# Kernel tuning notes

Hardware: AMD Instinct MI355X
Metric: run time of the kernel (lower is better)

The kernel has to match this reference:

```python
import jax, jax.numpy as jnp
import numpy as np

DIM = 1024
HEADS = 16
DIM_HEAD = 64
B = 16
N = 512
INNER = HEADS * DIM_HEAD            # 1024
CPB_DIM = DIM // 2                  # 512
INNER_FF = int(DIM * 4 * 2 / 3)     # 2730
EPS = 1e-5


def setup_inputs() -> dict:
    key = jax.random.key(0)
    ks = jax.random.split(key, 10)
    s = lambda i, shape, scale: jax.random.normal(ks[i], shape, jnp.float32) * scale
    return dict(
        x=s(0, (B, N, DIM), 1.0),
        g_ln=jnp.ones((DIM,), jnp.float32),
        Wq=s(1, (DIM, INNER), 0.02),
        Wkv=s(2, (DIM, 2 * INNER), 0.02),
        Wo=s(3, (INNER, DIM), 0.02),
        cpb_w1=s(4, (1, CPB_DIM), 0.5),
        cpb_b1=jnp.zeros((CPB_DIM,), jnp.float32),
        cpb_w2=s(5, (CPB_DIM, CPB_DIM), 0.05),
        cpb_b2=jnp.zeros((CPB_DIM,), jnp.float32),
        cpb_w3=s(6, (CPB_DIM, HEADS), 0.05),
        cpb_b3=jnp.zeros((HEADS,), jnp.float32),
        ff_w_in=s(7, (2 * INNER_FF, DIM), 0.02),
        ff_g=jnp.ones((INNER_FF,), jnp.float32),
        ff_w_out=s(8, (DIM, INNER_FF), 0.02),
    )


def _seq_ln(x, g):
    # Faithful to repo's LayerNorm: mean/var over dim=1 (sequence axis of [b,n,d])
    mean = jnp.mean(x, axis=1, keepdims=True)
    var = jnp.var(x, axis=1, keepdims=True)  # unbiased=False
    return (x - mean) * jax.lax.rsqrt(jnp.maximum(var, EPS)) * g


def reference(x, g_ln, Wq, Wkv, Wo, cpb_w1, cpb_b1, cpb_w2, cpb_b2, cpb_w3, cpb_b3,
              ff_w_in, ff_g, ff_w_out):
    b, n, d = x.shape
    # ContinuousPositionBias (1D, 2 layers)
    pos = jnp.arange(n, dtype=jnp.float32)
    rel = (pos[:, None] - pos[None, :])[..., None]           # [n,n,1]
    rel = jnp.sign(rel) * jnp.log(jnp.abs(rel) + 1.0)        # log-distance
    h = jax.nn.silu(rel @ cpb_w1 + cpb_b1)
    h = jax.nn.silu(h @ cpb_w2 + cpb_b2)
    bias = (h @ cpb_w3 + cpb_b3).transpose(2, 0, 1)          # [h,n,n]

    # Attention (framerate=None -> no pos_embeds; context = x)
    xn = _seq_ln(x, g_ln)
    q = xn @ Wq
    k, v = jnp.split(xn @ Wkv, 2, axis=-1)
    to_heads = lambda t: t.reshape(b, n, HEADS, DIM_HEAD).transpose(0, 2, 1, 3)
    q, k, v = to_heads(q), to_heads(k), to_heads(v)
    q = q * (DIM_HEAD ** -0.5)
    sim = jnp.einsum('bhid,bhjd->bhij', q, k) + bias[None]
    attn = jax.nn.softmax(sim, axis=-1)
    o = jnp.einsum('bhij,bhjd->bhid', attn, v)
    o = o.transpose(0, 2, 1, 3).reshape(b, n, INNER)
    x = jnp.nan_to_num(o @ Wo) + x

    # FeedForward: Conv1d(k=1) -> GEGLU -> ChanLayerNorm -> Conv1d(k=1), residual
    xt = x.transpose(0, 2, 1)                                # [b,d,n]
    hff = jnp.einsum('oc,bcn->bon', ff_w_in, xt)             # [b,2*inner_ff,n]
    x1, gate = jnp.split(hff, 2, axis=1)
    hff = x1 * jax.nn.gelu(gate, approximate=False)
    mean = jnp.mean(hff, axis=1, keepdims=True)
    var = jnp.var(hff, axis=1, keepdims=True)
    hff = (hff - mean) * jax.lax.rsqrt(jnp.maximum(var, EPS)) * ff_g[None, :, None]
    out = jnp.einsum('oc,bcn->bon', ff_w_out, hff).transpose(0, 2, 1) + x
    return out
```

## Files before the change

### kernel.cpp

```cpp
#include <hip/hip_runtime.h>

#define DEV __device__ __forceinline__

typedef __attribute__((ext_vector_type(8))) short bf16x8;
typedef __attribute__((ext_vector_type(4))) float f32x4;
typedef __attribute__((ext_vector_type(16))) float f32x16;

DEV float b2f(unsigned short u) { union { unsigned int i; float f; } v; v.i = ((unsigned)u) << 16; return v.f; }
DEV unsigned short f2b(float f) {
    union { float f; unsigned int i; } v; v.f = f;
    unsigned r = v.i + 0x7FFFu + ((v.i >> 16) & 1u);
    return (unsigned short)(r >> 16);
}

DEV void llds16(const unsigned short* g, unsigned short* l) {
    __builtin_amdgcn_global_load_lds((const __attribute__((address_space(1))) void*)g,
                                     (__attribute__((address_space(3))) void*)l, 16, 0, 0);
}

DEV float gelu_f(float x) {
    float y = 0.7978845608f * (x + 0.044715f * x * x * x);
    float th = 1.f - 2.f / (__expf(2.f * y) + 1.f);
    return 0.5f * x * (1.f + th);
}

__global__ __launch_bounds__(256) void transpose_cast_k(const float* __restrict__ src,
        unsigned short* __restrict__ dst, int Nc, int K, float scale)
{
    __shared__ float tile[32][33];
    int tx = threadIdx.x, ty = threadIdx.y;
    int c0 = blockIdx.x * 32;
    int r0 = blockIdx.y * 32;
#pragma unroll
    for (int r = 0; r < 4; r++)
        tile[ty + r * 8][tx] = src[(size_t)(r0 + ty + r * 8) * Nc + c0 + tx];
    __syncthreads();
#pragma unroll
    for (int r = 0; r < 4; r++)
        dst[(size_t)(c0 + ty + r * 8) * K + r0 + tx] = f2b(tile[tx][ty + r * 8] * scale);
}

__global__ __launch_bounds__(256) void cast_wfin_k(const float* __restrict__ src,
        unsigned short* __restrict__ dst)
{
    int idx = blockIdx.x * 256 + threadIdx.x;
    int nr = idx >> 8;
    int c4 = (idx & 255) * 4;
    int chunk = nr >> 6, which = (nr >> 5) & 1, pos = nr & 31;
    int c = chunk * 32 + pos;
    unsigned short o0 = 0, o1 = 0, o2 = 0, o3 = 0;
    if (c < 2730) {
        const float* s = src + (size_t)(which * 2730 + c) * 1024 + c4;
        o0 = f2b(s[0]); o1 = f2b(s[1]); o2 = f2b(s[2]); o3 = f2b(s[3]);
    }
    unsigned short* d = dst + (size_t)nr * 1024 + c4;
    d[0] = o0; d[1] = o1; d[2] = o2; d[3] = o3;
}

__global__ __launch_bounds__(256) void cast_wfoutg_k(const float* __restrict__ src,
        const float* __restrict__ g, unsigned short* __restrict__ dst)
{
    int idx = blockIdx.x * 256 + threadIdx.x;
    int r = idx / 2752, c = idx % 2752;
    float v = (c < 2730) ? src[(size_t)r * 2730 + c] * g[c] : 0.f;
    dst[idx] = f2b(v);
}

__global__ __launch_bounds__(64) void wgsum_k(const float* __restrict__ w,
        const float* __restrict__ g, float* __restrict__ wgs)
{
    int o = blockIdx.x, t = threadIdx.x;
    float s = 0.f;
    for (int c = t; c < 2730; c += 64) s += w[(size_t)o * 2730 + c] * g[c];
#pragma unroll
    for (int off = 32; off > 0; off >>= 1) s += __shfl_xor(s, off);
    if (t == 0) wgs[o] = s;
}

__global__ __launch_bounds__(512) void cpb_k(const float* __restrict__ w1, const float* __restrict__ b1,
        const float* __restrict__ w2, const float* __restrict__ b2,
        const float* __restrict__ w3, const float* __restrict__ b3,
        float* __restrict__ btbl)
{
    __shared__ float sH[512];
    __shared__ float sH2[512];
    int t = threadIdx.x, row = blockIdx.x;
    int dd = row - 511;
    float ad = fabsf((float)dd);
    float sgn = (dd > 0) ? 1.f : ((dd < 0) ? -1.f : 0.f);
    float rel = sgn * logf(ad + 1.f);
    float h1 = rel * w1[t] + b1[t];
    h1 = h1 / (1.f + __expf(-h1));
    sH[t] = h1;
    __syncthreads();
    float a = b2[t];
    for (int k = 0; k < 512; k++) a += sH[k] * w2[(size_t)k * 512 + t];
    a = a / (1.f + __expf(-a));
    sH2[t] = a;
    __syncthreads();
    if (t < 16) {
        float s = b3[t];
        for (int k = 0; k < 512; k++) s += sH2[k] * w3[k * 16 + t];
        btbl[t * 1023 + row] = s;
    }
}

__global__ __launch_bounds__(256) void ln_stat_k(const float* __restrict__ x,
        float* __restrict__ part_s, float* __restrict__ part_q)
{
    int b = blockIdx.x >> 4, nc = blockIdx.x & 15, t = threadIdx.x;
    const float* xp = x + ((size_t)b * 512 + nc * 32) * 1024;
#pragma unroll
    for (int dc = 0; dc < 4; dc++) {
        int d = dc * 256 + t;
        float s = 0.f, q = 0.f;
#pragma unroll 8
        for (int n = 0; n < 32; n++) { float v = xp[(size_t)n * 1024 + d]; s += v; q += v * v; }
        part_s[((size_t)b * 16 + nc) * 1024 + d] = s;
        part_q[((size_t)b * 16 + nc) * 1024 + d] = q;
    }
}

__global__ __launch_bounds__(256) void ln_reduce_k(const float* __restrict__ part_s,
        const float* __restrict__ part_q, const float* __restrict__ gln,
        float* __restrict__ mean, float* __restrict__ inv)
{
    int b = blockIdx.x >> 2, d = (blockIdx.x & 3) * 256 + threadIdx.x;
    float s = 0.f, q = 0.f;
#pragma unroll
    for (int c = 0; c < 16; c++) {
        s += part_s[((size_t)b * 16 + c) * 1024 + d];
        q += part_q[((size_t)b * 16 + c) * 1024 + d];
    }
    float m = s * (1.f / 512.f);
    float var = q * (1.f / 512.f) - m * m;
    mean[b * 1024 + d] = m;
    inv[b * 1024 + d] = rsqrtf(fmaxf(var, 1e-5f)) * gln[d];
}

__global__ __launch_bounds__(256) void ln_apply_k(const float* __restrict__ x,
        const float* __restrict__ mean, const float* __restrict__ inv,
        unsigned short* __restrict__ xn)
{
    int b = blockIdx.x >> 4, nc = blockIdx.x & 15, t = threadIdx.x;
    const float* xp = x + ((size_t)b * 512 + nc * 32) * 1024;
    unsigned short* op = xn + ((size_t)b * 512 + nc * 32) * 1024;
#pragma unroll
    for (int dc = 0; dc < 4; dc++) {
        int d = dc * 256 + t;
        float m = mean[b * 1024 + d], iv = inv[b * 1024 + d];
#pragma unroll 8
        for (int n = 0; n < 32; n++)
            op[(size_t)n * 1024 + d] = f2b((xp[(size_t)n * 1024 + d] - m) * iv);
    }
}

__global__ __launch_bounds__(256) void gemm_bt128_k(const unsigned short* __restrict__ A,
        const unsigned short* __restrict__ BT, unsigned short* __restrict__ C,
        float* __restrict__ OUTF, const float* __restrict__ RESF,
        const unsigned short* __restrict__ RESB,
        const float* __restrict__ MU, const float* __restrict__ INVV,
        const float* __restrict__ WGS, int K, int ldc, int mode)
{
    __shared__ __align__(16) unsigned short lds[16384];
    int t = threadIdx.x, lane = t & 63, w = t >> 6;
    int m0 = blockIdx.x * 128, n0 = blockIdx.y * 128;
    int wm = (w >> 1) * 64, wn = (w & 1) * 64;
    int lm = lane & 15, lq = lane >> 4;
    int srow = t >> 2, scol = (t & 3) * 8;
    const unsigned short* gA0 = A + (size_t)(m0 + srow) * K + scol;
    const unsigned short* gB0 = BT + (size_t)(n0 + srow) * K + scol;
    const size_t rstep = (size_t)64 * K;
    int wb = w * 512;

    f32x4 acc[4][4];
#pragma unroll
    for (int i = 0; i < 4; i++)
#pragma unroll
        for (int j = 0; j < 4; j++) acc[i][j] = (f32x4){0.f, 0.f, 0.f, 0.f};

    for (int kk = 0; kk < K; kk += 64) {
        __syncthreads();
        llds16(gA0 + kk,              &lds[wb]);
        llds16(gA0 + rstep + kk,      &lds[2048 + wb]);
        llds16(gB0 + kk,              &lds[4096 + wb]);
        llds16(gB0 + rstep + kk,      &lds[6144 + wb]);
        llds16(gA0 + kk + 32,         &lds[8192 + wb]);
        llds16(gA0 + rstep + kk + 32, &lds[10240 + wb]);
        llds16(gB0 + kk + 32,         &lds[12288 + wb]);
        llds16(gB0 + rstep + kk + 32, &lds[14336 + wb]);
        __syncthreads();
#pragma unroll
        for (int p = 0; p < 2; p++) {
            int pa = p * 8192, pb = p * 8192 + 4096;
            bf16x8 af[4], bfr[4];
#pragma unroll
            for (int i = 0; i < 4; i++) af[i] = *(const bf16x8*)&lds[pa + (wm + i * 16 + lm) * 32 + lq * 8];
#pragma unroll
            for (int j = 0; j < 4; j++) bfr[j] = *(const bf16x8*)&lds[pb + (wn + j * 16 + lm) * 32 + lq * 8];
#pragma unroll
            for (int i = 0; i < 4; i++)
#pragma unroll
                for (int j = 0; j < 4; j++)
                    acc[i][j] = __builtin_amdgcn_mfma_f32_16x16x32_bf16(af[i], bfr[j], acc[i][j], 0, 0, 0);
        }
    }

#pragma unroll
    for (int i = 0; i < 4; i++)
#pragma unroll
        for (int j = 0; j < 4; j++)
#pragma unroll
            for (int r = 0; r < 4; r++) {
                int row = m0 + wm + i * 16 + lq * 4 + r;
                int col = n0 + wn + j * 16 + lm;
                size_t idx = (size_t)row * ldc + col;
                float v = acc[i][j][r];
                if (mode == 1) { v += RESF[idx]; C[idx] = f2b(v); }
                if (mode == 2) {
                    float iv = INVV[row];
                    v = v * iv - MU[row] * iv * WGS[col] + b2f(RESB[idx]);
                    OUTF[idx] = v;
                }
            }
}

__global__ __launch_bounds__(256, 3) void gemm_bt256_k(const unsigned short* __restrict__ A,
        const unsigned short* __restrict__ BT, unsigned short* __restrict__ C, int K, int ldc)
{
    __shared__ __align__(16) unsigned short sL[24576];
    int t = threadIdx.x, lane = t & 63, w = t >> 6;
    int m0 = blockIdx.x * 256, n0 = blockIdx.y * 128;
    int wm = (w >> 1) * 128, wn = (w & 1) * 64;
    int l31 = lane & 31, lh = lane >> 5;
    int lrow4 = lane >> 2, lch = lane & 3;
    const unsigned short* gA = A + (size_t)(m0 + w * 64 + lrow4) * K + lch * 8;
    const unsigned short* gB = BT + (size_t)(n0 + w * 32 + lrow4) * K + lch * 8;

    f32x16 acc[4][2];
#pragma unroll
    for (int i = 0; i < 4; i++)
#pragma unroll
        for (int j = 0; j < 2; j++)
#pragma unroll
            for (int r = 0; r < 16; r++) acc[i][j][r] = 0.f;

    for (int kk = 0; kk < K; kk += 64) {
        __syncthreads();
#pragma unroll
        for (int c = 0; c < 4; c++)
            llds16(gA + (size_t)c * 16 * K + kk, &sL[(w * 4 + c) * 512]);
#pragma unroll
        for (int c = 0; c < 2; c++)
            llds16(gB + (size_t)c * 16 * K + kk, &sL[8192 + (w * 2 + c) * 512]);
#pragma unroll
        for (int c = 0; c < 4; c++)
            llds16(gA + (size_t)c * 16 * K + kk + 32, &sL[12288 + (w * 4 + c) * 512]);
#pragma unroll
        for (int c = 0; c < 2; c++)
            llds16(gB + (size_t)c * 16 * K + kk + 32, &sL[20480 + (w * 2 + c) * 512]);
        __syncthreads();
#pragma unroll
        for (int p = 0; p < 2; p++) {
            int pa = p * 12288, pb = p * 12288 + 8192;
#pragma unroll
            for (int s = 0; s < 2; s++) {
                int ko = s * 16 + lh * 8;
                bf16x8 af[4], bf[2];
#pragma unroll
                for (int i = 0; i < 4; i++)
                    af[i] = *(const bf16x8*)&sL[pa + (wm + i * 32 + l31) * 32 + ko];
#pragma unroll
                for (int j = 0; j < 2; j++)
                    bf[j] = *(const bf16x8*)&sL[pb + (wn + j * 32 + l31) * 32 + ko];
#pragma unroll
                for (int i = 0; i < 4; i++)
#pragma unroll
                    for (int j = 0; j < 2; j++)
                        acc[i][j] = __builtin_amdgcn_mfma_f32_32x32x16_bf16(af[i], bf[j], acc[i][j], 0, 0, 0);
            }
        }
    }

#pragma unroll
    for (int i = 0; i < 4; i++)
#pragma unroll
        for (int j = 0; j < 2; j++)
#pragma unroll
            for (int r = 0; r < 16; r++) {
                int row = m0 + wm + i * 32 + (r & 3) + 8 * (r >> 2) + 4 * lh;
                int col = n0 + wn + j * 32 + l31;
                C[(size_t)row * ldc + col] = f2b(acc[i][j][r]);
            }
}

__global__ __launch_bounds__(256, 3) void gemm_ffin_k(const unsigned short* __restrict__ A,
        const unsigned short* __restrict__ BT, unsigned short* __restrict__ HFFG, int K)
{
    __shared__ __align__(16) unsigned short sL[24576];
    int t = threadIdx.x, lane = t & 63, w = t >> 6;
    int m0 = blockIdx.x * 256, n0 = blockIdx.y * 128;
    int wm = (w >> 1) * 128, wn = (w & 1) * 64;
    int l31 = lane & 31, lh = lane >> 5;
    int lrow4 = lane >> 2, lch = lane & 3;
    const unsigned short* gA = A + (size_t)(m0 + w * 64 + lrow4) * K + lch * 8;
    const unsigned short* gB = BT + (size_t)(n0 + w * 32 + lrow4) * K + lch * 8;

    f32x16 acc[4][2];
#pragma unroll
    for (int i = 0; i < 4; i++)
#pragma unroll
        for (int j = 0; j < 2; j++)
#pragma unroll
            for (int r = 0; r < 16; r++) acc[i][j][r] = 0.f;

    for (int kk = 0; kk < K; kk += 64) {
        __syncthreads();
#pragma unroll
        for (int c = 0; c < 4; c++)
            llds16(gA + (size_t)c * 16 * K + kk, &sL[(w * 4 + c) * 512]);
#pragma unroll
        for (int c = 0; c < 2; c++)
            llds16(gB + (size_t)c * 16 * K + kk, &sL[8192 + (w * 2 + c) * 512]);
#pragma unroll
        for (int c = 0; c < 4; c++)
            llds16(gA + (size_t)c * 16 * K + kk + 32, &sL[12288 + (w * 4 + c) * 512]);
#pragma unroll
        for (int c = 0; c < 2; c++)
            llds16(gB + (size_t)c * 16 * K + kk + 32, &sL[20480 + (w * 2 + c) * 512]);
        __syncthreads();
#pragma unroll
        for (int p = 0; p < 2; p++) {
            int pa = p * 12288, pb = p * 12288 + 8192;
#pragma unroll
            for (int s = 0; s < 2; s++) {
                int ko = s * 16 + lh * 8;
                bf16x8 af[4], bf[2];
#pragma unroll
                for (int i = 0; i < 4; i++)
                    af[i] = *(const bf16x8*)&sL[pa + (wm + i * 32 + l31) * 32 + ko];
#pragma unroll
                for (int j = 0; j < 2; j++)
                    bf[j] = *(const bf16x8*)&sL[pb + (wn + j * 32 + l31) * 32 + ko];
#pragma unroll
                for (int i = 0; i < 4; i++)
#pragma unroll
                    for (int j = 0; j < 2; j++)
                        acc[i][j] = __builtin_amdgcn_mfma_f32_32x32x16_bf16(af[i], bf[j], acc[i][j], 0, 0, 0);
            }
        }
    }

    int c = (((n0 + wn) >> 6) << 5) + l31;
#pragma unroll
    for (int i = 0; i < 4; i++)
#pragma unroll
        for (int r = 0; r < 16; r++) {
            int row = m0 + wm + i * 32 + (r & 3) + 8 * (r >> 2) + 4 * lh;
            float x1 = acc[i][0][r];
            float gt = acc[i][1][r];
            HFFG[(size_t)row * 2752 + c] = f2b(x1 * gelu_f(gt));
        }
}

__global__ __launch_bounds__(256) void vtrans_k(const unsigned short* __restrict__ qkv,
        unsigned short* __restrict__ vT)
{
    __shared__ unsigned short sT[64 * 72];
    int t = threadIdx.x;
    int jt = blockIdx.x, bh = blockIdx.y;
    int b = bh >> 4, h = bh & 15;
#pragma unroll
    for (int it = 0; it < 16; it++) {
        int idx = it * 256 + t;
        int jl = idx >> 6, d = idx & 63;
        sT[d * 72 + jl] = qkv[((size_t)(b * 512 + jt * 64 + jl)) * 3072 + 2048 + h * 64 + d];
    }
    __syncthreads();
#pragma unroll
    for (int it = 0; it < 16; it++) {
        int idx = it * 256 + t;
        int d = idx >> 6, jl = idx & 63;
        vT[((size_t)(bh * 64 + d)) * 512 + jt * 64 + jl] = sT[d * 72 + jl];
    }
}

__global__ __launch_bounds__(256) void attn_k(const unsigned short* __restrict__ qkv,
        const unsigned short* __restrict__ vT, const float* __restrict__ btbl,
        unsigned short* __restrict__ attno)
{
    __shared__ __align__(16) unsigned short sQ[8192];
    __shared__ __align__(16) unsigned short sK[8192];
    __shared__ __align__(16) unsigned short sVT[8192];
    __shared__ __align__(16) unsigned short sP[8192];
    __shared__ float sB[1024];
    int t = threadIdx.x, lane = t & 63, w = t >> 6;
    int qt = blockIdx.x, h = blockIdx.y, b = blockIdx.z;
    int lm = lane & 15, lq = lane >> 4;
    int bh = b * 16 + h;
    int lrow4 = lane >> 2, lch = lane & 3;

    for (int i = t; i < 1023; i += 256) sB[i] = btbl[h * 1023 + i];

#pragma unroll
    for (int c = 0; c < 4; c++) {
        int cidx = w * 4 + c;
        int panel = cidx >> 3, r0 = (cidx & 7) * 16;
        const unsigned short* g = qkv + ((size_t)(b * 512 + qt * 128 + r0 + lrow4)) * 3072
                                  + h * 64 + panel * 32 + lch * 8;
        llds16(g, &sQ[panel * 4096 + r0 * 32]);
    }

    f32x4 o[2][4];
    float lrow[2][4];
#pragma unroll
    for (int it = 0; it < 2; it++)
#pragma unroll
        for (int z = 0; z < 4; z++) o[it][z] = (f32x4){0.f, 0.f, 0.f, 0.f};
#pragma unroll
    for (int it = 0; it < 2; it++)
#pragma unroll
        for (int r = 0; r < 4; r++) lrow[it][r] = 0.f;

    __syncthreads();

    bf16x8 aq[2][2];
#pragma unroll
    for (int it = 0; it < 2; it++)
#pragma unroll
        for (int kh = 0; kh < 2; kh++)
            aq[it][kh] = *(const bf16x8*)&sQ[kh * 4096 + (w * 32 + it * 16 + lm) * 32 + lq * 8];

    for (int jj = 0; jj < 4; jj++) {
        __syncthreads();
#pragma unroll
        for (int c = 0; c < 4; c++) {
            int cidx = w * 4 + c;
            int panel = cidx >> 3, r0 = (cidx & 7) * 16;
            const unsigned short* g = qkv + ((size_t)(b * 512 + jj * 128 + r0 + lrow4)) * 3072
                                      + 1024 + h * 64 + panel * 32 + lch * 8;
            llds16(g, &sK[panel * 4096 + r0 * 32]);
        }
#pragma unroll
        for (int c = 0; c < 4; c++) {
            int cidx = w * 4 + c;
            int panel = cidx >> 2, d0 = (cidx & 3) * 16;
            const unsigned short* g = vT + ((size_t)(bh * 64 + d0 + lrow4)) * 512
                                      + jj * 128 + panel * 32 + lch * 8;
            llds16(g, &sVT[panel * 2048 + d0 * 32]);
        }
        __syncthreads();

#pragma unroll
        for (int ch2 = 0; ch2 < 2; ch2++) {
            f32x4 s[2][4];
#pragma unroll
            for (int it = 0; it < 2; it++)
#pragma unroll
                for (int jt = 0; jt < 4; jt++) {
                    int jl = ch2 * 64 + jt * 16 + lm;
                    f32x4 c0 = {0.f, 0.f, 0.f, 0.f};
                    c0 = __builtin_amdgcn_mfma_f32_16x16x32_bf16(aq[it][0],
                            *(const bf16x8*)&sK[jl * 32 + lq * 8], c0, 0, 0, 0);
                    c0 = __builtin_amdgcn_mfma_f32_16x16x32_bf16(aq[it][1],
                            *(const bf16x8*)&sK[4096 + jl * 32 + lq * 8], c0, 0, 0, 0);
                    s[it][jt] = c0;
                }
            int jbase = jj * 128 + ch2 * 64;
#pragma unroll
            for (int it = 0; it < 2; it++) {
                int ibase = qt * 128 + w * 32 + it * 16;
#pragma unroll
                for (int r = 0; r < 4; r++) {
                    int ip = ibase + lq * 4 + r + 511 - jbase - lm;
                    float p0 = __expf(s[it][0][r] + sB[ip]);
                    float p1 = __expf(s[it][1][r] + sB[ip - 16]);
                    float p2 = __expf(s[it][2][r] + sB[ip - 32]);
                    float p3 = __expf(s[it][3][r] + sB[ip - 48]);
                    lrow[it][r] += (p0 + p1) + (p2 + p3);
                    int rowl = it * 16 + lq * 4 + r;
                    unsigned short* pp = &sP[w * 2048 + rowl * 64 + lm];
                    pp[0]  = f2b(p0);
                    pp[16] = f2b(p1);
                    pp[32] = f2b(p2);
                    pp[48] = f2b(p3);
                }
            }
#pragma unroll
            for (int it = 0; it < 2; it++)
#pragma unroll
                for (int kh = 0; kh < 2; kh++) {
                    bf16x8 ap = *(const bf16x8*)&sP[w * 2048 + (it * 16 + lm) * 64 + kh * 32 + lq * 8];
#pragma unroll
                    for (int dt = 0; dt < 4; dt++) {
                        bf16x8 bv = *(const bf16x8*)&sVT[(ch2 * 2 + kh) * 2048 + (dt * 16 + lm) * 32 + lq * 8];
                        o[it][dt] = __builtin_amdgcn_mfma_f32_16x16x32_bf16(ap, bv, o[it][dt], 0, 0, 0);
                    }
                }
        }
    }

#pragma unroll
    for (int it = 0; it < 2; it++)
#pragma unroll
        for (int r = 0; r < 4; r++) {
            float tot = lrow[it][r];
#pragma unroll
            for (int off = 8; off > 0; off >>= 1) tot += __shfl_xor(tot, off);
            float inv = 1.f / tot;
            int row = b * 512 + qt * 128 + w * 32 + it * 16 + lq * 4 + r;
#pragma unroll
            for (int dt = 0; dt < 4; dt++)
                attno[(size_t)row * 1024 + h * 64 + dt * 16 + lm] = f2b(o[it][dt][r] * inv);
        }
}

__global__ __launch_bounds__(256) void chstat_k(const unsigned short* __restrict__ hffg,
        float* __restrict__ mu, float* __restrict__ inv)
{
    int row = blockIdx.x, t = threadIdx.x;
    const unsigned short* rp = hffg + (size_t)row * 2752;
    float sum = 0.f, ss = 0.f;
    for (int v8 = t; v8 < 344; v8 += 256) {
        bf16x8 x = *(const bf16x8*)&rp[v8 * 8];
#pragma unroll
        for (int e = 0; e < 8; e++) {
            float f = b2f((unsigned short)x[e]);
            sum += f; ss += f * f;
        }
    }
#pragma unroll
    for (int off = 32; off > 0; off >>= 1) { sum += __shfl_xor(sum, off); ss += __shfl_xor(ss, off); }
    __shared__ float rb[8];
    int w = t >> 6;
    if ((t & 63) == 0) { rb[w] = sum; rb[4 + w] = ss; }
    __syncthreads();
    if (t == 0) {
        sum = rb[0] + rb[1] + rb[2] + rb[3];
        ss = rb[4] + rb[5] + rb[6] + rb[7];
        float m = sum * (1.f / 2730.f);
        float var = ss * (1.f / 2730.f) - m * m;
        mu[row] = m;
        inv[row] = rsqrtf(fmaxf(var, 1e-5f));
    }
}

extern "C" void kernel_launch(void* const* d_in, const int* in_sizes, int n_in,
                              void* d_out, int out_size, void* d_ws, size_t ws_size,
                              hipStream_t stream) {
    const float* x      = (const float*)d_in[0];
    const float* g_ln   = (const float*)d_in[1];
    const float* Wq     = (const float*)d_in[2];
    const float* Wkv    = (const float*)d_in[3];
    const float* Wo     = (const float*)d_in[4];
    const float* cw1    = (const float*)d_in[5];
    const float* cb1    = (const float*)d_in[6];
    const float* cw2    = (const float*)d_in[7];
    const float* cb2    = (const float*)d_in[8];
    const float* cw3    = (const float*)d_in[9];
    const float* cb3    = (const float*)d_in[10];
    const float* ffwin  = (const float*)d_in[11];
    const float* ffg    = (const float*)d_in[12];
    const float* ffwout = (const float*)d_in[13];

    char* ws = (char*)d_ws;
    unsigned short* xn    = (unsigned short*)(ws + 0);
    unsigned short* wqkvT = (unsigned short*)(ws + 16777216);
    unsigned short* woT   = (unsigned short*)(ws + 23068672);
    unsigned short* qkv   = (unsigned short*)(ws + 25165824);
    unsigned short* vT    = (unsigned short*)(ws + 75497472);
    unsigned short* attno = (unsigned short*)(ws + 92274688);
    unsigned short* hffg  = (unsigned short*)(ws + 0);
    unsigned short* wfin  = (unsigned short*)(ws + 109051904);
    unsigned short* wfout = (unsigned short*)(ws + 120324096);
    float*          btbl  = (float*)(ws + 125960192);
    unsigned short* x2b   = (unsigned short*)(ws + 126025728);
    float*          part_s = (float*)(ws + 142802944);
    float*          part_q = (float*)(ws + 143851520);
    float*          lnmean = (float*)(ws + 144900096);
    float*          lninv  = (float*)(ws + 144965632);
    float*          chmu   = (float*)(ws + 145031168);
    float*          chinv  = (float*)(ws + 145063936);
    float*          wgs    = (float*)(ws + 145096704);

    dim3 tb(32, 8);
    transpose_cast_k<<<dim3(32, 32), tb, 0, stream>>>(Wq, wqkvT, 1024, 1024, 0.125f);
    transpose_cast_k<<<dim3(64, 32), tb, 0, stream>>>(Wkv, wqkvT + (size_t)1024 * 1024, 2048, 1024, 1.0f);
    transpose_cast_k<<<dim3(32, 32), tb, 0, stream>>>(Wo, woT, 1024, 1024, 1.0f);
    cast_wfin_k<<<5504, 256, 0, stream>>>(ffwin, wfin);
    cast_wfoutg_k<<<11008, 256, 0, stream>>>(ffwout, ffg, wfout);
    wgsum_k<<<1024, 64, 0, stream>>>(ffwout, ffg, wgs);
    cpb_k<<<1023, 512, 0, stream>>>(cw1, cb1, cw2, cb2, cw3, cb3, btbl);
    ln_stat_k<<<256, 256, 0, stream>>>(x, part_s, part_q);
    ln_reduce_k<<<64, 256, 0, stream>>>(part_s, part_q, g_ln, lnmean, lninv);
    ln_apply_k<<<256, 256, 0, stream>>>(x, lnmean, lninv, xn);
    gemm_bt256_k<<<dim3(32, 24), 256, 0, stream>>>(xn, wqkvT, qkv, 1024, 3072);
    vtrans_k<<<dim3(8, 256), 256, 0, stream>>>(qkv, vT);
    attn_k<<<dim3(4, 16, 16), 256, 0, stream>>>(qkv, vT, btbl, attno);
    gemm_bt128_k<<<dim3(64, 8), 256, 0, stream>>>(attno, woT, x2b, nullptr, x, nullptr,
                                                  nullptr, nullptr, nullptr, 1024, 1024, 1);
    gemm_ffin_k<<<dim3(32, 43), 256, 0, stream>>>(x2b, wfin, hffg, 1024);
    chstat_k<<<8192, 256, 0, stream>>>(hffg, chmu, chinv);
    gemm_bt128_k<<<dim3(64, 8), 256, 0, stream>>>(hffg, wfout, nullptr, (float*)d_out, nullptr, x2b,
                                                  chmu, chinv, wgs, 2752, 1024, 2);
}
```

Measured before the change: 594.2 us.

## Replace QKV and FF-in GEMMs with 256x256 double-buffered 8-wave pipelined kernel

Replaces the two 256x128 single-buffered GEMM kernels with one templated 512-thread kernel that computes 256x256 tiles using 16x16x32 MFMAs. It double-buffers LDS with XOR-swizzled layout, interleaves global->LDS prefetch of the next K tile with MFMA quadrants, uses s_setprio around MFMA bursts, and swizzles block IDs for L2 locality. The aim is to hide load latency behind compute and raise arithmetic intensity. The trade-offs are 128KB of LDS per block, clamped B rows for the ragged FF-in N dimension, and hardcoded K=1024 strides.

```diff
diff --git a/kernel.cpp b/kernel.cpp
--- a/kernel.cpp
+++ b/kernel.cpp
@@ -4,7 +4,6 @@
 
 typedef __attribute__((ext_vector_type(8))) short bf16x8;
 typedef __attribute__((ext_vector_type(4))) float f32x4;
-typedef __attribute__((ext_vector_type(16))) float f32x16;
 
 DEV float b2f(unsigned short u) { union { unsigned int i; float f; } v; v.i = ((unsigned)u) << 16; return v.f; }
 DEV unsigned short f2b(float f) {
@@ -225,143 +224,153 @@
             }
 }
 
-__global__ __launch_bounds__(256, 3) void gemm_bt256_k(const unsigned short* __restrict__ A,
-        const unsigned short* __restrict__ BT, unsigned short* __restrict__ C, int K, int ldc)
-{
-    __shared__ __align__(16) unsigned short sL[24576];
+
+#define RDA8(AF, MH, BUF) { \
+    _Pragma("unroll") \
+    for (int i_ = 0; i_ < 4; i_++) { \
+        AF[i_][0] = *(const bf16x8*)(sc8 + (BUF) + rbA + (MH) * 8192 + i_ * 2048 + soff0); \
+        AF[i_][1] = *(const bf16x8*)(sc8 + (BUF) + rbA + (MH) * 8192 + i_ * 2048 + soff1); \
+    } }
+#define RDB8(BF, NH, BUF) { \
+    _Pragma("unroll") \
+    for (int j_ = 0; j_ < 2; j_++) { \
+        BF[j_][0] = *(const bf16x8*)(sc8 + (BUF) + 32768 + rbB + (NH) * 4096 + j_ * 2048 + soff0); \
+        BF[j_][1] = *(const bf16x8*)(sc8 + (BUF) + 32768 + rbB + (NH) * 4096 + j_ * 2048 + soff1); \
+    } }
+#define MFQ8(MH, NH, AF, BF) { \
+    __builtin_amdgcn_s_setprio(1); \
+    _Pragma("unroll") \
+    for (int i_ = 0; i_ < 4; i_++) { \
+        _Pragma("unroll") \
+        for (int j_ = 0; j_ < 2; j_++) { \
+            acc[(MH) * 4 + i_][(NH) * 2 + j_] = __builtin_amdgcn_mfma_f32_16x16x32_bf16( \
+                AF[i_][0], BF[j_][0], acc[(MH) * 4 + i_][(NH) * 2 + j_], 0, 0, 0); \
+            acc[(MH) * 4 + i_][(NH) * 2 + j_] = __builtin_amdgcn_mfma_f32_16x16x32_bf16( \
+                AF[i_][1], BF[j_][1], acc[(MH) * 4 + i_][(NH) * 2 + j_], 0, 0, 0); \
+        } } \
+    __builtin_amdgcn_s_setprio(0); }
+#define STGA8(BUF, H, KE) do { \
+    llds16(A + oA[(H) * 2] + (KE),     &sL[((BUF) + (H) * 16384 + wst) >> 1]); \
+    llds16(A + oA[(H) * 2 + 1] + (KE), &sL[((BUF) + (H) * 16384 + 8192 + wst) >> 1]); \
+} while (0)
+#define STGB8(BUF, H, KE) do { \
+    llds16(BT + oB[(H) * 2] + (KE),     &sL[((BUF) + 32768 + (H) * 16384 + wst) >> 1]); \
+    llds16(BT + oB[(H) * 2 + 1] + (KE), &sL[((BUF) + 32768 + (H) * 16384 + 8192 + wst) >> 1]); \
+} while (0)
+#define TILE8(TTV, DO_A, DO_B2, LASTW) { \
+    int bufc_ = ((TTV) & 1) << 16; \
+    int bufn_ = bufc_ ^ 65536; \
+    int kA1_ = ((TTV) + 1) * 64; \
+    int kB2_ = ((TTV) + 2) * 64; \
+    (void)bufn_; (void)kA1_; (void)kB2_; \
+    bf16x8 a0[4][2], a1[4][2], b0[2][2], b1[2][2]; \
+    RDA8(a0, 0, bufc_); \
+    RDB8(b0, 0, bufc_); \
+    if (DO_A) STGA8(bufn_, 0, kA1_); \
+    __builtin_amdgcn_s_barrier(); \
+    MFQ8(0, 0, a0, b0); \
+    __builtin_amdgcn_s_barrier(); \
+    RDB8(b1, 1, bufc_); \
+    if (DO_A) STGA8(bufn_, 1, kA1_); \
+    __builtin_amdgcn_s_barrier(); \
+    MFQ8(0, 1, a0, b1); \
+    __builtin_amdgcn_s_barrier(); \
+    RDA8(a1, 1, bufc_); \
+    if (DO_B2) STGB8(bufc_, 0, kB2_); \
+    __builtin_amdgcn_s_barrier(); \
+    MFQ8(1, 0, a1, b0); \
+    __builtin_amdgcn_s_barrier(); \
+    if (DO_B2) STGB8(bufc_, 1, kB2_); \
+    __builtin_amdgcn_s_barrier(); \
+    MFQ8(1, 1, a1, b1); \
+    if ((LASTW) == 4) asm volatile("s_waitcnt vmcnt(4)" ::: "memory"); \
+    if ((LASTW) == 0) asm volatile("s_waitcnt vmcnt(0)" ::: "memory"); \
+    __builtin_amdgcn_s_barrier(); \
+}
+
+template<int MODE, int NTILES>
+__global__ __launch_bounds__(512, 2) void g8_k(const unsigned short* __restrict__ A,
+        const unsigned short* __restrict__ BT, unsigned short* __restrict__ OUT,
+        int NB, int ldc)
+{
+    __shared__ __align__(16) unsigned short sL[65536];
+    const char* sc8 = (const char*)sL;
     int t = threadIdx.x, lane = t & 63, w = t >> 6;
-    int m0 = blockIdx.x * 256, n0 = blockIdx.y * 128;
-    int wm = (w >> 1) * 128, wn = (w & 1) * 64;
-    int l31 = lane & 31, lh = lane >> 5;
-    int lrow4 = lane >> 2, lch = lane & 3;
-    const unsigned short* gA = A + (size_t)(m0 + w * 64 + lrow4) * K + lch * 8;
-    const unsigned short* gB = BT + (size_t)(n0 + w * 32 + lrow4) * K + lch * 8;
-
-    f32x16 acc[4][2];
-#pragma unroll
-    for (int i = 0; i < 4; i++)
-#pragma unroll
-        for (int j = 0; j < 2; j++)
-#pragma unroll
-            for (int r = 0; r < 16; r++) acc[i][j][r] = 0.f;
-
-    for (int kk = 0; kk < K; kk += 64) {
-        __syncthreads();
-#pragma unroll
-        for (int c = 0; c < 4; c++)
-            llds16(gA + (size_t)c * 16 * K + kk, &sL[(w * 4 + c) * 512]);
-#pragma unroll
-        for (int c = 0; c < 2; c++)
-            llds16(gB + (size_t)c * 16 * K + kk, &sL[8192 + (w * 2 + c) * 512]);
-#pragma unroll
-        for (int c = 0; c < 4; c++)
-            llds16(gA + (size_t)c * 16 * K + kk + 32, &sL[12288 + (w * 4 + c) * 512]);
-#pragma unroll
-        for (int c = 0; c < 2; c++)
-            llds16(gB + (size_t)c * 16 * K + kk + 32, &sL[20480 + (w * 2 + c) * 512]);
-        __syncthreads();
-#pragma unroll
-        for (int p = 0; p < 2; p++) {
-            int pa = p * 12288, pb = p * 12288 + 8192;
-#pragma unroll
-            for (int s = 0; s < 2; s++) {
-                int ko = s * 16 + lh * 8;
-                bf16x8 af[4], bf[2];
-#pragma unroll
-                for (int i = 0; i < 4; i++)
-                    af[i] = *(const bf16x8*)&sL[pa + (wm + i * 32 + l31) * 32 + ko];
-#pragma unroll
-                for (int j = 0; j < 2; j++)
-                    bf[j] = *(const bf16x8*)&sL[pb + (wn + j * 32 + l31) * 32 + ko];
-#pragma unroll
-                for (int i = 0; i < 4; i++)
-#pragma unroll
-                    for (int j = 0; j < 2; j++)
-                        acc[i][j] = __builtin_amdgcn_mfma_f32_32x32x16_bf16(af[i], bf[j], acc[i][j], 0, 0, 0);
-            }
+    int cpx = gridDim.x >> 3;
+    int bid = blockIdx.x;
+    int swz = (bid & 7) * cpx + (bid >> 3);
+    int m0 = (swz & 31) * 256, n0 = (swz >> 5) * 256;
+    int wm = (w >> 2) * 128, wn = (w & 3) * 64;
+    int lm = lane & 15, lq = lane >> 4;
+    int rbA = wm * 128, rbB = wn * 128;
+    int soff0 = lm * 128 + ((lq ^ (lm & 7)) << 4);
+    int soff1 = lm * 128 + (((4 | lq) ^ (lm & 7)) << 4);
+    int wst = w * 1024;
+    int sr = t >> 3;
+    int scw = ((t & 7) ^ (sr & 7)) << 3;
+    int oA[4], oB[4];
+#pragma unroll
+    for (int hp = 0; hp < 4; hp++) {
+        oA[hp] = (m0 + hp * 64 + sr) * 1024 + scw;
+        int rb = n0 + hp * 64 + sr;
+        if (rb > NB - 1) rb = NB - 1;
+        oB[hp] = rb * 1024 + scw;
+    }
+
+    f32x4 acc[8][4];
+#pragma unroll
+    for (int i = 0; i < 8; i++)
+#pragma unroll
+        for (int j = 0; j < 4; j++) acc[i][j] = (f32x4){0.f, 0.f, 0.f, 0.f};
+
+    STGB8(0, 0, 0);
+    STGB8(0, 1, 0);
+    STGA8(0, 0, 0);
+    STGA8(0, 1, 0);
+    STGB8(65536, 0, 64);
+    STGB8(65536, 1, 64);
+    asm volatile("s_waitcnt vmcnt(4)" ::: "memory");
+    __builtin_amdgcn_s_barrier();
+
+#pragma unroll 2
+    for (int tt = 0; tt < NTILES - 2; tt++) TILE8(tt, 1, 1, 4);
+    TILE8(NTILES - 2, 1, 0, 0);
+    TILE8(NTILES - 1, 0, 0, -1);
+
+    if (MODE == 0) {
+#pragma unroll
+        for (int i = 0; i < 8; i++)
+#pragma unroll
+            for (int j = 0; j < 4; j++)
+#pragma unroll
+                for (int r = 0; r < 4; r++) {
+                    int row = m0 + wm + i * 16 + lq * 4 + r;
+                    int col = n0 + wn + j * 16 + lm;
+                    OUT[(size_t)row * ldc + col] = f2b(acc[i][j][r]);
+                }
+    } else {
+        int chunk = (n0 + wn) >> 6;
+        if (chunk < 86) {
+#pragma unroll
+            for (int i = 0; i < 8; i++)
+#pragma unroll
+                for (int jp = 0; jp < 2; jp++)
+#pragma unroll
+                    for (int r = 0; r < 4; r++) {
+                        int row = m0 + wm + i * 16 + lq * 4 + r;
+                        int c = chunk * 32 + jp * 16 + lm;
+                        OUT[(size_t)row * 2752 + c] = f2b(acc[i][jp][r] * gelu_f(acc[i][jp + 2][r]));
+                    }
         }
     }
-
-#pragma unroll
-    for (int i = 0; i < 4; i++)
-#pragma unroll
-        for (int j = 0; j < 2; j++)
-#pragma unroll
-            for (int r = 0; r < 16; r++) {
-                int row = m0 + wm + i * 32 + (r & 3) + 8 * (r >> 2) + 4 * lh;
-                int col = n0 + wn + j * 32 + l31;
-                C[(size_t)row * ldc + col] = f2b(acc[i][j][r]);
-            }
-}
-
-__global__ __launch_bounds__(256, 3) void gemm_ffin_k(const unsigned short* __restrict__ A,
-        const unsigned short* __restrict__ BT, unsigned short* __restrict__ HFFG, int K)
-{
-    __shared__ __align__(16) unsigned short sL[24576];
-    int t = threadIdx.x, lane = t & 63, w = t >> 6;
-    int m0 = blockIdx.x * 256, n0 = blockIdx.y * 128;
-    int wm = (w >> 1) * 128, wn = (w & 1) * 64;
-    int l31 = lane & 31, lh = lane >> 5;
-    int lrow4 = lane >> 2, lch = lane & 3;
-    const unsigned short* gA = A + (size_t)(m0 + w * 64 + lrow4) * K + lch * 8;
-    const unsigned short* gB = BT + (size_t)(n0 + w * 32 + lrow4) * K + lch * 8;
-
-    f32x16 acc[4][2];
-#pragma unroll
-    for (int i = 0; i < 4; i++)
-#pragma unroll
-        for (int j = 0; j < 2; j++)
-#pragma unroll
-            for (int r = 0; r < 16; r++) acc[i][j][r] = 0.f;
-
-    for (int kk = 0; kk < K; kk += 64) {
-        __syncthreads();
-#pragma unroll
-        for (int c = 0; c < 4; c++)
-            llds16(gA + (size_t)c * 16 * K + kk, &sL[(w * 4 + c) * 512]);
-#pragma unroll
-        for (int c = 0; c < 2; c++)
-            llds16(gB + (size_t)c * 16 * K + kk, &sL[8192 + (w * 2 + c) * 512]);
-#pragma unroll
-        for (int c = 0; c < 4; c++)
-            llds16(gA + (size_t)c * 16 * K + kk + 32, &sL[12288 + (w * 4 + c) * 512]);
-#pragma unroll
-        for (int c = 0; c < 2; c++)
-            llds16(gB + (size_t)c * 16 * K + kk + 32, &sL[20480 + (w * 2 + c) * 512]);
-        __syncthreads();
-#pragma unroll
-        for (int p = 0; p < 2; p++) {
-            int pa = p * 12288, pb = p * 12288 + 8192;
-#pragma unroll
-            for (int s = 0; s < 2; s++) {
-                int ko = s * 16 + lh * 8;
-                bf16x8 af[4], bf[2];
-#pragma unroll
-                for (int i = 0; i < 4; i++)
-                    af[i] = *(const bf16x8*)&sL[pa + (wm + i * 32 + l31) * 32 + ko];
-#pragma unroll
-                for (int j = 0; j < 2; j++)
-                    bf[j] = *(const bf16x8*)&sL[pb + (wn + j * 32 + l31) * 32 + ko];
-#pragma unroll
-                for (int i = 0; i < 4; i++)
-#pragma unroll
-                    for (int j = 0; j < 2; j++)
-                        acc[i][j] = __builtin_amdgcn_mfma_f32_32x32x16_bf16(af[i], bf[j], acc[i][j], 0, 0, 0);
-            }
-        }
-    }
-
-    int c = (((n0 + wn) >> 6) << 5) + l31;
-#pragma unroll
-    for (int i = 0; i < 4; i++)
-#pragma unroll
-        for (int r = 0; r < 16; r++) {
-            int row = m0 + wm + i * 32 + (r & 3) + 8 * (r >> 2) + 4 * lh;
-            float x1 = acc[i][0][r];
-            float gt = acc[i][1][r];
-            HFFG[(size_t)row * 2752 + c] = f2b(x1 * gelu_f(gt));
-        }
-}
+}
+
+#undef RDA8
+#undef RDB8
+#undef MFQ8
+#undef STGA8
+#undef STGB8
+#undef TILE8
 
 __global__ __launch_bounds__(256) void vtrans_k(const unsigned short* __restrict__ qkv,
         unsigned short* __restrict__ vT)
@@ -594,12 +603,12 @@
     ln_stat_k<<<256, 256, 0, stream>>>(x, part_s, part_q);
     ln_reduce_k<<<64, 256, 0, stream>>>(part_s, part_q, g_ln, lnmean, lninv);
     ln_apply_k<<<256, 256, 0, stream>>>(x, lnmean, lninv, xn);
-    gemm_bt256_k<<<dim3(32, 24), 256, 0, stream>>>(xn, wqkvT, qkv, 1024, 3072);
+    g8_k<0, 16><<<dim3(384), 512, 0, stream>>>(xn, wqkvT, qkv, 3072, 3072);
     vtrans_k<<<dim3(8, 256), 256, 0, stream>>>(qkv, vT);
     attn_k<<<dim3(4, 16, 16), 256, 0, stream>>>(qkv, vT, btbl, attno);
     gemm_bt128_k<<<dim3(64, 8), 256, 0, stream>>>(attno, woT, x2b, nullptr, x, nullptr,
                                                   nullptr, nullptr, nullptr, 1024, 1024, 1);
-    gemm_ffin_k<<<dim3(32, 43), 256, 0, stream>>>(x2b, wfin, hffg, 1024);
+    g8_k<1, 16><<<dim3(704), 512, 0, stream>>>(x2b, wfin, hffg, 5504, 0);
     chstat_k<<<8192, 256, 0, stream>>>(hffg, chmu, chinv);
     gemm_bt128_k<<<dim3(64, 8), 256, 0, stream>>>(hffg, wfout, nullptr, (float*)d_out, nullptr, x2b,
                                                   chmu, chinv, wgs, 2752, 1024, 2);
```

New measurement: 583.2 us. Within noise of the previous version (-1.9%).
